# Performance work log

Hardware: AMD Instinct MI355X
Metric: run time of the kernel (lower is better)

Reference implementation:

```python
import jax, jax.numpy as jnp
import numpy as np

D_MODEL = 512
N_HEADS = 8
D_HEAD = D_MODEL // N_HEADS
N_LAYERS = 6
VOCAB = 32000
B, S = 4, 1024
EPS = 1e-5


def positional_encoding(length, d_model):
    # matches get_positional_encoding_table: pos * (1/10000**(i/d)), sin on even i, cos on odd i
    inv = 1.0 / (10000.0 ** (jnp.arange(d_model, dtype=jnp.float32) / d_model))
    ang = jnp.arange(length, dtype=jnp.float32)[:, None] * inv[None, :]  # [S, D]
    pe = jnp.where(jnp.arange(d_model) % 2 == 0, jnp.sin(ang), jnp.cos(ang))
    return pe


def layer_norm(x, g, b):
    m = jnp.mean(x, axis=-1, keepdims=True)
    v = jnp.mean((x - m) ** 2, axis=-1, keepdims=True)
    return (x - m) * jax.lax.rsqrt(v + EPS) * g + b


def setup_inputs() -> dict:
    key = jax.random.key(0)
    ks = jax.random.split(key, 9)
    sc = 0.02
    return {
        "tokens": jax.random.randint(ks[0], (B, S), 0, VOCAB),
        "emb": jax.random.normal(ks[1], (VOCAB, D_MODEL), jnp.float32) * sc,
        "Wq": jax.random.normal(ks[2], (N_LAYERS, D_MODEL, D_MODEL), jnp.float32) * sc,
        "bq": jnp.zeros((N_LAYERS, D_MODEL), jnp.float32),
        "Wk": jax.random.normal(ks[3], (N_LAYERS, D_MODEL, D_MODEL), jnp.float32) * sc,
        "bk": jnp.zeros((N_LAYERS, D_MODEL), jnp.float32),
        "Wv": jax.random.normal(ks[4], (N_LAYERS, D_MODEL, D_MODEL), jnp.float32) * sc,
        "bv": jnp.zeros((N_LAYERS, D_MODEL), jnp.float32),
        "Wo": jax.random.normal(ks[5], (N_LAYERS, D_MODEL, D_MODEL), jnp.float32) * sc,
        "bo": jnp.zeros((N_LAYERS, D_MODEL), jnp.float32),
        "W1": jax.random.normal(ks[6], (N_LAYERS, D_MODEL, 4 * D_MODEL), jnp.float32) * sc,
        "b1": jnp.zeros((N_LAYERS, 4 * D_MODEL), jnp.float32),
        "W2": jax.random.normal(ks[7], (N_LAYERS, 4 * D_MODEL, D_MODEL), jnp.float32) * sc,
        "b2": jnp.zeros((N_LAYERS, D_MODEL), jnp.float32),
        "ln_g": jnp.ones((N_LAYERS, D_MODEL), jnp.float32),
        "ln_b": jnp.zeros((N_LAYERS, D_MODEL), jnp.float32),
    }


def encoder_layer(x, Wq, bq, Wk, bk, Wv, bv, Wo, bo, W1, b1, W2, b2, g, b):
    bsz = x.shape[0]
    q = (x @ Wq + bq).reshape(bsz, -1, N_HEADS, D_HEAD).transpose(0, 2, 1, 3)  # [B,h,S,dk]
    k = (x @ Wk + bk).reshape(bsz, -1, N_HEADS, D_HEAD).transpose(0, 2, 1, 3)
    v = (x @ Wv + bv).reshape(bsz, -1, N_HEADS, D_HEAD).transpose(0, 2, 1, 3)
    scores = jnp.einsum('bhqd,bhkd->bhqk', q, k) / (D_HEAD ** 0.5)
    w = jax.nn.softmax(scores, axis=-1)
    attn = jnp.einsum('bhqk,bhkd->bhqd', w, v)  # [B,h,S,dv]
    # faithful to source bug: .view(B,-1,h*dv) WITHOUT transposing heads back
    attn = attn.reshape(bsz, -1, N_HEADS * D_HEAD)  # [B,S,D] with heads/seq interleaved
    x = layer_norm(x + (attn @ Wo + bo), g, b)
    ffn = jnp.maximum(x @ W1 + b1, 0.0) @ W2 + b2
    x = layer_norm(x + ffn, g, b)  # same (shared) LayerNorm params, as in source
    return x


def reference(tokens, emb, Wq, bq, Wk, bk, Wv, bv, Wo, bo, W1, b1, W2, b2, ln_g, ln_b):
    x = emb[tokens]  # [B,S,D]
    x = x + positional_encoding(x.shape[1], D_MODEL)
    for i in range(N_LAYERS):
        x = encoder_layer(x, Wq[i], bq[i], Wk[i], bk[i], Wv[i], bv[i], Wo[i], bo[i],
                          W1[i], b1[i], W2[i], b2[i], ln_g[i], ln_b[i])
    return x
```

## Files before the change

kernel.cpp:

```cpp
#include <hip/hip_runtime.h>
#include <hip/hip_bf16.h>
#include <math.h>

typedef unsigned short ushort_t;
typedef unsigned int uint_t;
typedef __attribute__((ext_vector_type(8))) short bfrag_t;
typedef __attribute__((ext_vector_type(4))) float facc_t;
typedef __attribute__((ext_vector_type(16))) float facc16_t;

#define D_MODEL 512
#define NH 8
#define DH 64
#define NL 6
#define BB 4
#define SS 1024
#define ROWS (BB*SS)
#define DFF 2048

__device__ inline ushort_t f2bf(float f) {
    __hip_bfloat16 h = __float2bfloat16(f);
    return *(ushort_t*)&h;
}
__device__ inline float bf2f(ushort_t u) {
    unsigned int x = ((unsigned int)u) << 16;
    union { unsigned int i; float f; } c; c.i = x;
    return c.f;
}
__device__ inline uint_t pkbf(float lo, float hi) {
    return (uint_t)f2bf(lo) | ((uint_t)f2bf(hi) << 16);
}
__device__ inline void gload_lds16(const void* g, void* l) {
    __builtin_amdgcn_global_load_lds((const __attribute__((address_space(1))) unsigned int*)g,
                                     (__attribute__((address_space(3))) unsigned int*)l, 16, 0, 0);
}

__global__ __launch_bounds__(256) void embed_pe(const int* __restrict__ tok,
                                                const float* __restrict__ emb,
                                                float* __restrict__ x,
                                                ushort_t* __restrict__ xbf) {
    int row = blockIdx.x;
    int s = row & (SS - 1);
    int t = tok[row];
    const float* e = emb + (size_t)t * D_MODEL;
    for (int i = threadIdx.x; i < D_MODEL; i += 256) {
        float freq = __expf(-9.210340371976184f * ((float)i / (float)D_MODEL));
        float ang = (float)s * freq;
        float pe = (i & 1) ? cosf(ang) : sinf(ang);
        float v = e[i] + pe;
        x[(size_t)row * D_MODEL + i] = v;
        xbf[(size_t)row * D_MODEL + i] = f2bf(v);
    }
}

__global__ __launch_bounds__(256) void prep_weights(const float* __restrict__ Wq,
                                                    const float* __restrict__ Wk,
                                                    const float* __restrict__ Wv,
                                                    const float* __restrict__ Wo,
                                                    const float* __restrict__ W1,
                                                    const float* __restrict__ W2,
                                                    int layer, ushort_t* __restrict__ wlay) {
    __shared__ float tile[32][33];
    int z = blockIdx.z;
    const float* src; ushort_t* dst; int K, N;
    size_t o512 = (size_t)layer * 512 * 512;
    size_t o1M  = (size_t)layer * 512 * 2048;
    switch (z) {
        case 0: src = Wq + o512; dst = wlay;               K = 512;  N = 512;  break;
        case 1: src = Wk + o512; dst = wlay + 262144;      K = 512;  N = 512;  break;
        case 2: src = Wv + o512; dst = wlay + 524288;      K = 512;  N = 512;  break;
        case 3: src = Wo + o512; dst = wlay + 786432;      K = 512;  N = 512;  break;
        case 4: src = W1 + o1M;  dst = wlay + 1048576;     K = 512;  N = 2048; break;
        default:src = W2 + o1M;  dst = wlay + 2097152;     K = 2048; N = 512;  break;
    }
    int n0 = blockIdx.x * 32, k0 = blockIdx.y * 32;
    if (n0 >= N || k0 >= K) return;
    int tx = threadIdx.x & 31, ty = threadIdx.x >> 5;
    #pragma unroll
    for (int i = 0; i < 4; i++)
        tile[ty + i * 8][tx] = src[(size_t)(k0 + ty + i * 8) * N + n0 + tx];
    __syncthreads();
    #pragma unroll
    for (int i = 0; i < 4; i++)
        dst[(size_t)(n0 + ty + i * 8) * K + k0 + tx] = f2bf(tile[tx][ty + i * 8]);
}

__global__ __launch_bounds__(256) void concat_bias(const float* __restrict__ bq,
                                                   const float* __restrict__ bk,
                                                   const float* __restrict__ bv,
                                                   float* __restrict__ bqkv) {
    int l = blockIdx.x;
    for (int i = threadIdx.x; i < 1536; i += 256) {
        float v = (i < 512) ? bq[l * 512 + i]
                : (i < 1024) ? bk[l * 512 + i - 512]
                : bv[l * 512 + i - 1024];
        bqkv[l * 1536 + i] = v;
    }
}

template<int BM, int BN, int SPLIT>
__global__ __launch_bounds__(256) void gemm_pipe(const ushort_t* __restrict__ A,
                                                 const ushort_t* __restrict__ Bt,
                                                 const float* __restrict__ bias,
                                                 float* __restrict__ Cf,
                                                 ushort_t* __restrict__ Cb0,
                                                 ushort_t* __restrict__ Cb1,
                                                 int N, int Ktot, int relu) {
    constexpr int TI = BM / 32, TJ = BN / 32;
    __shared__ ushort_t lA[2][BM * 64];
    __shared__ ushort_t lB[2][BN * 64];

    const int tid = threadIdx.x;
    const int w = tid >> 6, lane = tid & 63;
    const int wr = w & 1, wc = w >> 1;
    const int lane16 = lane & 15, quad = lane >> 4;
    const int row0 = blockIdx.y * BM, col0 = blockIdx.x * BN;
    const int kz = (SPLIT > 1) ? blockIdx.z : 0;
    const int Ks = Ktot / SPLIT;
    const int kbeg = kz * Ks;

    facc_t acc[TI][TJ];
    #pragma unroll
    for (int i = 0; i < TI; i++)
        #pragma unroll
        for (int j = 0; j < TJ; j++)
            acc[i][j] = (facc_t){0.f, 0.f, 0.f, 0.f};

    auto stage = [&](int buf, int k0) {
        #pragma unroll
        for (int i = 0; i < BM / 32; i++) {
            int g = i * 256 + tid;
            int r = g >> 3, p = g & 7;
            int q = p ^ (r & 7);
            gload_lds16(A + (size_t)(row0 + r) * Ktot + kbeg + k0 + q * 8,
                        lA[buf] + (size_t)g * 8);
        }
        #pragma unroll
        for (int i = 0; i < BN / 32; i++) {
            int g = i * 256 + tid;
            int r = g >> 3, p = g & 7;
            int q = p ^ (r & 7);
            gload_lds16(Bt + (size_t)(col0 + r) * Ktot + kbeg + k0 + q * 8,
                        lB[buf] + (size_t)g * 8);
        }
    };
    auto compute = [&](int buf) {
        #pragma unroll
        for (int kk = 0; kk < 2; kk++) {
            bfrag_t af[TI], bf_[TJ];
            int q = kk * 4 + quad;
            #pragma unroll
            for (int t = 0; t < TI; t++) {
                int m = wr * (BM / 2) + t * 16 + lane16;
                af[t] = *(const bfrag_t*)(lA[buf] + ((size_t)m * 8 + (q ^ (m & 7))) * 8);
            }
            #pragma unroll
            for (int t = 0; t < TJ; t++) {
                int n = wc * (BN / 2) + t * 16 + lane16;
                bf_[t] = *(const bfrag_t*)(lB[buf] + ((size_t)n * 8 + (q ^ (n & 7))) * 8);
            }
            #pragma unroll
            for (int ti = 0; ti < TI; ti++)
                #pragma unroll
                for (int tj = 0; tj < TJ; tj++)
                    acc[ti][tj] = __builtin_amdgcn_mfma_f32_16x16x32_bf16(
                        af[ti], bf_[tj], acc[ti][tj], 0, 0, 0);
        }
    };

    const int nt = Ks >> 6;
    stage(0, 0);
    __syncthreads();
    for (int t = 0; t < nt; t++) {
        if (t + 1 < nt) stage((t + 1) & 1, (t + 1) * 64);
        compute(t & 1);
        __syncthreads();
    }

    float bv_[TJ];
    #pragma unroll
    for (int tj = 0; tj < TJ; tj++)
        bv_[tj] = (SPLIT > 1 && kz != 0) ? 0.f
                 : bias[col0 + wc * (BN / 2) + tj * 16 + lane16];

    ushort_t* Cb = (SPLIT > 1 && kz != 0) ? Cb1 : Cb0;

    #pragma unroll
    for (int ti = 0; ti < TI; ti++) {
        int grow = row0 + wr * (BM / 2) + ti * 16 + quad * 4;
        #pragma unroll
        for (int tj = 0; tj < TJ; tj++) {
            int gcol = col0 + wc * (BN / 2) + tj * 16 + lane16;
            #pragma unroll
            for (int rr = 0; rr < 4; rr++) {
                float v = acc[ti][tj][rr] + bv_[tj];
                if (relu) v = fmaxf(v, 0.f);
                size_t idx = (size_t)(grow + rr) * N + gcol;
                if (Cf) Cf[idx] = v;
                if (Cb) Cb[idx] = f2bf(v);
            }
        }
    }
}

__global__ __launch_bounds__(128) void attn_mfma_split(const ushort_t* __restrict__ qkv,
                                                       ushort_t* __restrict__ Yp,
                                                       float2* __restrict__ mlp) {
    __shared__ __align__(16) ushort_t lK[4096];
    __shared__ __align__(16) ushort_t lVT[2][4096];

    const int tid = threadIdx.x;
    const int w = tid >> 6, lane = tid & 63;
    const int l31 = lane & 31, H = lane >> 5;
    const int qt = blockIdx.x, h = blockIdx.y;
    const int b = blockIdx.z >> 1, kh = blockIdx.z & 1;
    const int kt0 = kh * 8;

    const float LOG2E = 1.4426950408889634f;
    const float SC = 0.125f * 1.4426950408889634f;

    const ushort_t* Qrow = qkv + (size_t)(b * SS + qt * 64 + w * 32 + l31) * 1536 + h * 64;
    bfrag_t qb[4];
    #pragma unroll
    for (int s = 0; s < 4; s++)
        qb[s] = *(const bfrag_t*)(Qrow + s * 16 + H * 8);

    facc16_t O0, O1;
    #pragma unroll
    for (int r = 0; r < 16; r++) { O0[r] = 0.f; O1[r] = 0.f; }
    float mrow = -INFINITY, lrow = 0.f;

    const int vkey = tid & 63;
    const int vdg  = tid >> 6;
    const int vk8 = vkey >> 3, vj = vkey & 7;

    auto stageK = [&](int kt) {
        #pragma unroll
        for (int i = 0; i < 4; i++) {
            int g = i * 128 + tid;
            int r = g >> 3, p = g & 7;
            int q = p ^ (r & 7);
            gload_lds16(qkv + (size_t)(b * SS + kt * 64 + r) * 1536 + h * 64 + 512 + q * 8,
                        lK + (size_t)g * 8);
        }
    };
    auto loadV = [&](int kt, ushort_t* vs) {
        const ushort_t* vsrc = qkv + (size_t)(b * SS + kt * 64 + vkey) * 1536
                               + h * 64 + 1024 + vdg * 32;
        #pragma unroll
        for (int i4 = 0; i4 < 4; i4++)
            *(uint4*)(vs + i4 * 8) = *(const uint4*)(vsrc + i4 * 8);
    };
    auto writeV = [&](const ushort_t* vs, int buf) {
        #pragma unroll
        for (int e = 0; e < 32; e++) {
            int n = vdg * 32 + e;
            lVT[buf][(size_t)(n * 8 + (vk8 ^ (n & 7))) * 8 + vj] = vs[e];
        }
    };

    {
        ushort_t v0[32];
        stageK(kt0);
        loadV(kt0, v0);
        writeV(v0, 0);
    }
    __syncthreads();

    for (int kt = kt0; kt < kt0 + 8; kt++) {
        const int buf = (kt - kt0) & 1;
        const bool more = (kt < kt0 + 7);

        ushort_t vn[32];
        if (more) loadV(kt + 1, vn);

        facc16_t sfv[2];
        #pragma unroll
        for (int half = 0; half < 2; half++) {
            facc16_t s_;
            #pragma unroll
            for (int r = 0; r < 16; r++) s_[r] = 0.f;
            int row = half * 32 + l31;
            #pragma unroll
            for (int s = 0; s < 4; s++) {
                int c = 2 * s + H;
                bfrag_t kf = *(const bfrag_t*)(lK + ((size_t)row * 8 + (c ^ (row & 7))) * 8);
                s_ = __builtin_amdgcn_mfma_f32_32x32x16_bf16(kf, qb[s], s_, 0, 0, 0);
            }
            sfv[half] = s_;
        }

        if (more) {
            __syncthreads();
            stageK(kt + 1);
        }

        #pragma unroll
        for (int half = 0; half < 2; half++) {
            facc16_t s_ = sfv[half];

            float mt = s_[0];
            #pragma unroll
            for (int r = 1; r < 16; r++) mt = fmaxf(mt, s_[r]);
            mt *= 0.125f;
            mt = fmaxf(mt, __shfl_xor(mt, 32));

            bool small = (mt <= mrow + 8.f);
            if (!__all(small)) {
                float mn = fmaxf(mrow, mt);
                float al = __builtin_amdgcn_exp2f((mrow - mn) * LOG2E);
                mrow = mn;
                lrow *= al;
                #pragma unroll
                for (int r = 0; r < 16; r++) { O0[r] *= al; O1[r] *= al; }
            }
            float mC = mrow * LOG2E;

            float p[16];
            float ps = 0.f;
            #pragma unroll
            for (int r = 0; r < 16; r++) {
                p[r] = __builtin_amdgcn_exp2f(fmaf(s_[r], SC, -mC));
                ps += p[r];
            }
            ps += __shfl_xor(ps, 32);
            lrow += ps;

            uint_t A0 = pkbf(p[0], p[1]),   A1 = pkbf(p[2], p[3]);
            uint_t B0 = pkbf(p[4], p[5]),   B1 = pkbf(p[6], p[7]);
            uint_t C0 = pkbf(p[8], p[9]),   C1 = pkbf(p[10], p[11]);
            uint_t D0 = pkbf(p[12], p[13]), D1 = pkbf(p[14], p[15]);
            uint_t XA0 = __shfl_xor(A0, 32), XA1 = __shfl_xor(A1, 32);
            uint_t XB0 = __shfl_xor(B0, 32), XB1 = __shfl_xor(B1, 32);
            uint_t XC0 = __shfl_xor(C0, 32), XC1 = __shfl_xor(C1, 32);
            uint_t XD0 = __shfl_xor(D0, 32), XD1 = __shfl_xor(D1, 32);

            union { bfrag_t v; uint_t u[4]; } pf0, pf1;
            pf0.u[0] = H ? XB0 : A0;  pf0.u[1] = H ? XB1 : A1;
            pf0.u[2] = H ? B0 : XA0;  pf0.u[3] = H ? B1 : XA1;
            pf1.u[0] = H ? XD0 : C0;  pf1.u[1] = H ? XD1 : C1;
            pf1.u[2] = H ? D0 : XC0;  pf1.u[3] = H ? D1 : XC1;

            #pragma unroll
            for (int t = 0; t < 2; t++) {
                int n = 32 * t + l31;
                #pragma unroll
                for (int ks = 0; ks < 2; ks++) {
                    int c = half * 4 + 2 * ks + H;
                    bfrag_t vf = *(const bfrag_t*)(&lVT[buf][((size_t)n * 8 + (c ^ (n & 7))) * 8]);
                    if (t == 0)
                        O0 = __builtin_amdgcn_mfma_f32_32x32x16_bf16(
                            vf, ks ? pf1.v : pf0.v, O0, 0, 0, 0);
                    else
                        O1 = __builtin_amdgcn_mfma_f32_32x32x16_bf16(
                            vf, ks ? pf1.v : pf0.v, O1, 0, 0, 0);
                }
            }
        }

        if (more) writeV(vn, buf ^ 1);

        __syncthreads();
    }

    size_t rbase = ((size_t)(kh * BB + b) * NH + h) * SS + qt * 64 + w * 32 + l31;
    float inv = 1.f / lrow;
    #pragma unroll
    for (int t = 0; t < 2; t++) {
        #pragma unroll
        for (int g = 0; g < 4; g++) {
            float v0 = (t ? O1[4 * g]     : O0[4 * g])     * inv;
            float v1 = (t ? O1[4 * g + 1] : O0[4 * g + 1]) * inv;
            float v2 = (t ? O1[4 * g + 2] : O0[4 * g + 2]) * inv;
            float v3 = (t ? O1[4 * g + 3] : O0[4 * g + 3]) * inv;
            uint2 pkd = make_uint2(pkbf(v0, v1), pkbf(v2, v3));
            *(uint2*)(Yp + rbase * DH + 32 * t + 8 * g + 4 * H) = pkd;
        }
    }
    if (H == 0)
        mlp[rbase] = make_float2(mrow, lrow);
}

__global__ __launch_bounds__(256) void attn_combine(const ushort_t* __restrict__ Yp,
                                                    const float2* __restrict__ mlp,
                                                    ushort_t* __restrict__ ab) {
    const float LOG2E = 1.4426950408889634f;
    int rid = blockIdx.x * 32 + (threadIdx.x >> 3);
    int d0 = (threadIdx.x & 7) * 8;
    float2 ml0 = mlp[rid];
    float2 ml1 = mlp[32768 + rid];
    float m = fmaxf(ml0.x, ml1.x);
    float a0 = __builtin_amdgcn_exp2f((ml0.x - m) * LOG2E) * ml0.y;
    float a1 = __builtin_amdgcn_exp2f((ml1.x - m) * LOG2E) * ml1.y;
    float inv = 1.f / (a0 + a1);
    a0 *= inv; a1 *= inv;
    uint4 u0 = *(const uint4*)(Yp + (size_t)rid * DH + d0);
    uint4 u1 = *(const uint4*)(Yp + (size_t)32768 * DH + (size_t)rid * DH + d0);
    const ushort_t* p0 = (const ushort_t*)&u0;
    const ushort_t* p1 = (const ushort_t*)&u1;
    ushort_t o[8];
    #pragma unroll
    for (int e = 0; e < 8; e++)
        o[e] = f2bf(a0 * bf2f(p0[e]) + a1 * bf2f(p1[e]));
    *(uint4*)(ab + (size_t)rid * DH + d0) = *(uint4*)o;
}

template<int NP>
__global__ __launch_bounds__(256) void add_lnb(const float* __restrict__ x,
                                               const ushort_t* __restrict__ d0,
                                               const ushort_t* __restrict__ d1,
                                               const float* __restrict__ g,
                                               const float* __restrict__ bparm,
                                               float* __restrict__ outf,
                                               ushort_t* __restrict__ outb) {
    __shared__ float red[2][4];
    int row = blockIdx.x;
    int t = threadIdx.x;
    const float* xr = x + (size_t)row * D_MODEL;
    const ushort_t* dr0 = d0 + (size_t)row * D_MODEL;
    float del0 = bf2f(dr0[t]);
    float del1 = bf2f(dr0[t + 256]);
    if (NP == 2) {
        const ushort_t* dr1 = d1 + (size_t)row * D_MODEL;
        del0 += bf2f(dr1[t]);
        del1 += bf2f(dr1[t + 256]);
    }
    float v0 = xr[t] + del0;
    float v1 = xr[t + 256] + del1;
    float s = v0 + v1;
    float ss = v0 * v0 + v1 * v1;
    #pragma unroll
    for (int off = 1; off < 64; off <<= 1) {
        s  += __shfl_xor(s, off);
        ss += __shfl_xor(ss, off);
    }
    int lane = t & 63, wid = t >> 6;
    if (lane == 0) { red[0][wid] = s; red[1][wid] = ss; }
    __syncthreads();
    s  = red[0][0] + red[0][1] + red[0][2] + red[0][3];
    ss = red[1][0] + red[1][1] + red[1][2] + red[1][3];
    float mean = s * (1.f / D_MODEL);
    float var = ss * (1.f / D_MODEL) - mean * mean;
    float rinv = rsqrtf(var + 1e-5f);
    float o0 = (v0 - mean) * rinv * g[t]       + bparm[t];
    float o1 = (v1 - mean) * rinv * g[t + 256] + bparm[t + 256];
    float* orow = outf + (size_t)row * D_MODEL;
    orow[t] = o0; orow[t + 256] = o1;
    ushort_t* brow = outb + (size_t)row * D_MODEL;
    brow[t] = f2bf(o0); brow[t + 256] = f2bf(o1);
}

extern "C" void kernel_launch(void* const* d_in, const int* in_sizes, int n_in,
                              void* d_out, int out_size, void* d_ws, size_t ws_size,
                              hipStream_t stream) {
    const int* tokens = (const int*)d_in[0];
    const float* emb = (const float*)d_in[1];
    const float* Wq = (const float*)d_in[2];  const float* bq = (const float*)d_in[3];
    const float* Wk = (const float*)d_in[4];  const float* bk = (const float*)d_in[5];
    const float* Wv = (const float*)d_in[6];  const float* bv = (const float*)d_in[7];
    const float* Wo = (const float*)d_in[8];  const float* bo = (const float*)d_in[9];
    const float* W1 = (const float*)d_in[10]; const float* b1 = (const float*)d_in[11];
    const float* W2 = (const float*)d_in[12]; const float* b2 = (const float*)d_in[13];
    const float* lng = (const float*)d_in[14]; const float* lnb = (const float*)d_in[15];

    char* base = (char*)d_ws;
    ushort_t* wlay = (ushort_t*)(base);
    float*    bqkv = (float*)   (base + 6291456);
    float*    x    = (float*)   (base + 6328320);
    ushort_t* xbf  = (ushort_t*)(base + 14716928);
    float*    tmp  = (float*)   (base + 18911232);
    ushort_t* qkv  = (ushort_t*)(base + 27299840);
    ushort_t* ab   = (ushort_t*)(base + 39882752);
    ushort_t* mid  = qkv;

    ushort_t* Yp   = (ushort_t*)tmp;
    float2*   mlp  = (float2*)xbf;
    ushort_t* dlt0 = (ushort_t*)tmp;
    ushort_t* dlt1 = (ushort_t*)tmp + 2097152;

    ushort_t* wqkv_t = wlay;
    ushort_t* wo_t   = wlay + 786432;
    ushort_t* w1_t   = wlay + 1048576;
    ushort_t* w2_t   = wlay + 2097152;

    concat_bias<<<NL, 256, 0, stream>>>(bq, bk, bv, bqkv);
    embed_pe<<<ROWS, 256, 0, stream>>>(tokens, emb, x, xbf);

    for (int l = 0; l < NL; l++) {
        prep_weights<<<dim3(64, 64, 6), 256, 0, stream>>>(Wq, Wk, Wv, Wo, W1, W2, l, wlay);

        gemm_pipe<128, 64, 1><<<dim3(24, 32), 256, 0, stream>>>(
            xbf, wqkv_t, bqkv + l * 1536, nullptr, qkv, nullptr, 1536, 512, 0);

        attn_mfma_split<<<dim3(16, NH, BB * 2), 128, 0, stream>>>(qkv, Yp, mlp);
        attn_combine<<<1024, 256, 0, stream>>>(Yp, mlp, ab);

        gemm_pipe<64, 64, 1><<<dim3(8, 64), 256, 0, stream>>>(
            ab, wo_t, bo + l * D_MODEL, nullptr, dlt0, nullptr, 512, 512, 0);
        add_lnb<1><<<ROWS, 256, 0, stream>>>(x, dlt0, nullptr,
                                             lng + l * D_MODEL, lnb + l * D_MODEL,
                                             x, xbf);

        gemm_pipe<128, 128, 1><<<dim3(16, 32), 256, 0, stream>>>(
            xbf, w1_t, b1 + l * DFF, nullptr, mid, nullptr, 2048, 512, 1);

        gemm_pipe<64, 64, 2><<<dim3(8, 64, 2), 256, 0, stream>>>(
            mid, w2_t, b2 + l * D_MODEL, nullptr, dlt0, dlt1, 512, 2048, 0);

        float* lnout = (l == NL - 1) ? (float*)d_out : x;
        add_lnb<2><<<ROWS, 256, 0, stream>>>(x, dlt0, dlt1,
                                             lng + l * D_MODEL, lnb + l * D_MODEL,
                                             lnout, xbf);
    }
}
```

Before: 856.5 us.

## Split attention key range four ways and combine partials in a four-way merge

After: 887.2 us. +3.6%, slower.

```diff
diff --git a/kernel.cpp b/kernel.cpp
--- a/kernel.cpp
+++ b/kernel.cpp
@@ -202,18 +202,21 @@
     }
 }
 
-__global__ __launch_bounds__(128) void attn_mfma_split(const ushort_t* __restrict__ qkv,
-                                                       ushort_t* __restrict__ Yp,
-                                                       float2* __restrict__ mlp) {
+__global__ __launch_bounds__(128) void attn_mfma_split4(const ushort_t* __restrict__ qkv,
+                                                        ushort_t* __restrict__ Yp0,
+                                                        ushort_t* __restrict__ Yp1,
+                                                        ushort_t* __restrict__ Yp2,
+                                                        ushort_t* __restrict__ Yp3,
+                                                        float2* __restrict__ mlp) {
     __shared__ __align__(16) ushort_t lK[4096];
-    __shared__ __align__(16) ushort_t lVT[2][4096];
+    __shared__ __align__(16) ushort_t lVT[4096];
 
     const int tid = threadIdx.x;
     const int w = tid >> 6, lane = tid & 63;
     const int l31 = lane & 31, H = lane >> 5;
     const int qt = blockIdx.x, h = blockIdx.y;
-    const int b = blockIdx.z >> 1, kh = blockIdx.z & 1;
-    const int kt0 = kh * 8;
+    const int b = blockIdx.z >> 2, kh = blockIdx.z & 3;
+    const int kt0 = kh * 4;
 
     const float LOG2E = 1.4426950408889634f;
     const float SC = 0.125f * 1.4426950408889634f;
@@ -250,11 +253,11 @@
         for (int i4 = 0; i4 < 4; i4++)
             *(uint4*)(vs + i4 * 8) = *(const uint4*)(vsrc + i4 * 8);
     };
-    auto writeV = [&](const ushort_t* vs, int buf) {
+    auto writeV = [&](const ushort_t* vs) {
         #pragma unroll
         for (int e = 0; e < 32; e++) {
             int n = vdg * 32 + e;
-            lVT[buf][(size_t)(n * 8 + (vk8 ^ (n & 7))) * 8 + vj] = vs[e];
+            lVT[(size_t)(n * 8 + (vk8 ^ (n & 7))) * 8 + vj] = vs[e];
         }
     };
 
@@ -262,18 +265,18 @@
         ushort_t v0[32];
         stageK(kt0);
         loadV(kt0, v0);
-        writeV(v0, 0);
+        writeV(v0);
     }
     __syncthreads();
 
-    for (int kt = kt0; kt < kt0 + 8; kt++) {
-        const int buf = (kt - kt0) & 1;
-        const bool more = (kt < kt0 + 7);
+    for (int kt = kt0; kt < kt0 + 4; kt++) {
+        const bool more = (kt < kt0 + 3);
 
         ushort_t vn[32];
         if (more) loadV(kt + 1, vn);
 
         facc16_t sfv[2];
+        __builtin_amdgcn_s_setprio(1);
         #pragma unroll
         for (int half = 0; half < 2; half++) {
             facc16_t s_;
@@ -288,6 +291,7 @@
             }
             sfv[half] = s_;
         }
+        __builtin_amdgcn_s_setprio(0);
 
         if (more) {
             __syncthreads();
@@ -298,10 +302,12 @@
         for (int half = 0; half < 2; half++) {
             facc16_t s_ = sfv[half];
 
-            float mt = s_[0];
-            #pragma unroll
-            for (int r = 1; r < 16; r++) mt = fmaxf(mt, s_[r]);
-            mt *= 0.125f;
+            float t0 = fmaxf(s_[0], s_[1]),   t1 = fmaxf(s_[2], s_[3]);
+            float t2 = fmaxf(s_[4], s_[5]),   t3 = fmaxf(s_[6], s_[7]);
+            float t4 = fmaxf(s_[8], s_[9]),   t5 = fmaxf(s_[10], s_[11]);
+            float t6 = fmaxf(s_[12], s_[13]), t7 = fmaxf(s_[14], s_[15]);
+            float mt = fmaxf(fmaxf(fmaxf(t0, t1), fmaxf(t2, t3)),
+                             fmaxf(fmaxf(t4, t5), fmaxf(t6, t7))) * 0.125f;
             mt = fmaxf(mt, __shfl_xor(mt, 32));
 
             bool small = (mt <= mrow + 8.f);
@@ -316,12 +322,14 @@
             float mC = mrow * LOG2E;
 
             float p[16];
-            float ps = 0.f;
-            #pragma unroll
-            for (int r = 0; r < 16; r++) {
+            #pragma unroll
+            for (int r = 0; r < 16; r++)
                 p[r] = __builtin_amdgcn_exp2f(fmaf(s_[r], SC, -mC));
-                ps += p[r];
-            }
+            float u0 = p[0] + p[1],   u1 = p[2] + p[3];
+            float u2 = p[4] + p[5],   u3 = p[6] + p[7];
+            float u4 = p[8] + p[9],   u5 = p[10] + p[11];
+            float u6 = p[12] + p[13], u7 = p[14] + p[15];
+            float ps = ((u0 + u1) + (u2 + u3)) + ((u4 + u5) + (u6 + u7));
             ps += __shfl_xor(ps, 32);
             lrow += ps;
 
@@ -340,13 +348,14 @@
             pf1.u[0] = H ? XD0 : C0;  pf1.u[1] = H ? XD1 : C1;
             pf1.u[2] = H ? D0 : XC0;  pf1.u[3] = H ? D1 : XC1;
 
+            __builtin_amdgcn_s_setprio(1);
             #pragma unroll
             for (int t = 0; t < 2; t++) {
                 int n = 32 * t + l31;
                 #pragma unroll
                 for (int ks = 0; ks < 2; ks++) {
                     int c = half * 4 + 2 * ks + H;
-                    bfrag_t vf = *(const bfrag_t*)(&lVT[buf][((size_t)n * 8 + (c ^ (n & 7))) * 8]);
+                    bfrag_t vf = *(const bfrag_t*)(lVT + ((size_t)n * 8 + (c ^ (n & 7))) * 8);
                     if (t == 0)
                         O0 = __builtin_amdgcn_mfma_f32_32x32x16_bf16(
                             vf, ks ? pf1.v : pf0.v, O0, 0, 0, 0);
@@ -355,14 +364,17 @@
                             vf, ks ? pf1.v : pf0.v, O1, 0, 0, 0);
                 }
             }
-        }
-
-        if (more) writeV(vn, buf ^ 1);
-
-        __syncthreads();
-    }
-
-    size_t rbase = ((size_t)(kh * BB + b) * NH + h) * SS + qt * 64 + w * 32 + l31;
+            __builtin_amdgcn_s_setprio(0);
+        }
+
+        if (more) {
+            __syncthreads();
+            writeV(vn);
+        }
+    }
+
+    ushort_t* Ypz = (kh == 0) ? Yp0 : (kh == 1) ? Yp1 : (kh == 2) ? Yp2 : Yp3;
+    size_t rbase = ((size_t)b * NH + h) * SS + qt * 64 + w * 32 + l31;
     float inv = 1.f / lrow;
     #pragma unroll
     for (int t = 0; t < 2; t++) {
@@ -373,35 +385,48 @@
             float v2 = (t ? O1[4 * g + 2] : O0[4 * g + 2]) * inv;
             float v3 = (t ? O1[4 * g + 3] : O0[4 * g + 3]) * inv;
             uint2 pkd = make_uint2(pkbf(v0, v1), pkbf(v2, v3));
-            *(uint2*)(Yp + rbase * DH + 32 * t + 8 * g + 4 * H) = pkd;
+            *(uint2*)(Ypz + rbase * DH + 32 * t + 8 * g + 4 * H) = pkd;
         }
     }
     if (H == 0)
-        mlp[rbase] = make_float2(mrow, lrow);
-}
-
-__global__ __launch_bounds__(256) void attn_combine(const ushort_t* __restrict__ Yp,
-                                                    const float2* __restrict__ mlp,
-                                                    ushort_t* __restrict__ ab) {
+        mlp[(size_t)kh * 32768 + rbase] = make_float2(mrow, lrow);
+}
+
+__global__ __launch_bounds__(256) void attn_combine4(const ushort_t* __restrict__ Y0,
+                                                     const ushort_t* __restrict__ Y1,
+                                                     const ushort_t* __restrict__ Y2,
+                                                     const ushort_t* __restrict__ Y3,
+                                                     const float2* __restrict__ mlp,
+                                                     ushort_t* __restrict__ ab) {
     const float LOG2E = 1.4426950408889634f;
     int rid = blockIdx.x * 32 + (threadIdx.x >> 3);
     int d0 = (threadIdx.x & 7) * 8;
     float2 ml0 = mlp[rid];
     float2 ml1 = mlp[32768 + rid];
-    float m = fmaxf(ml0.x, ml1.x);
+    float2 ml2 = mlp[65536 + rid];
+    float2 ml3 = mlp[98304 + rid];
+    float m = fmaxf(fmaxf(ml0.x, ml1.x), fmaxf(ml2.x, ml3.x));
     float a0 = __builtin_amdgcn_exp2f((ml0.x - m) * LOG2E) * ml0.y;
     float a1 = __builtin_amdgcn_exp2f((ml1.x - m) * LOG2E) * ml1.y;
-    float inv = 1.f / (a0 + a1);
-    a0 *= inv; a1 *= inv;
-    uint4 u0 = *(const uint4*)(Yp + (size_t)rid * DH + d0);
-    uint4 u1 = *(const uint4*)(Yp + (size_t)32768 * DH + (size_t)rid * DH + d0);
+    float a2 = __builtin_amdgcn_exp2f((ml2.x - m) * LOG2E) * ml2.y;
+    float a3 = __builtin_amdgcn_exp2f((ml3.x - m) * LOG2E) * ml3.y;
+    float inv = 1.f / (((a0 + a1) + (a2 + a3)));
+    a0 *= inv; a1 *= inv; a2 *= inv; a3 *= inv;
+    size_t off = (size_t)rid * DH + d0;
+    uint4 u0 = *(const uint4*)(Y0 + off);
+    uint4 u1 = *(const uint4*)(Y1 + off);
+    uint4 u2 = *(const uint4*)(Y2 + off);
+    uint4 u3 = *(const uint4*)(Y3 + off);
     const ushort_t* p0 = (const ushort_t*)&u0;
     const ushort_t* p1 = (const ushort_t*)&u1;
+    const ushort_t* p2 = (const ushort_t*)&u2;
+    const ushort_t* p3 = (const ushort_t*)&u3;
     ushort_t o[8];
     #pragma unroll
     for (int e = 0; e < 8; e++)
-        o[e] = f2bf(a0 * bf2f(p0[e]) + a1 * bf2f(p1[e]));
-    *(uint4*)(ab + (size_t)rid * DH + d0) = *(uint4*)o;
+        o[e] = f2bf((a0 * bf2f(p0[e]) + a1 * bf2f(p1[e]))
+                  + (a2 * bf2f(p2[e]) + a3 * bf2f(p3[e])));
+    *(uint4*)(ab + off) = *(uint4*)o;
 }
 
 template<int NP>
@@ -472,8 +497,11 @@
     ushort_t* ab   = (ushort_t*)(base + 39882752);
     ushort_t* mid  = qkv;
 
-    ushort_t* Yp   = (ushort_t*)tmp;
-    float2*   mlp  = (float2*)xbf;
+    ushort_t* Yp0  = (ushort_t*)tmp;
+    ushort_t* Yp1  = (ushort_t*)tmp + 2097152;
+    ushort_t* Yp2  = ab;
+    ushort_t* Yp3  = xbf;
+    float2*   mlp  = (float2*)wlay;
     ushort_t* dlt0 = (ushort_t*)tmp;
     ushort_t* dlt1 = (ushort_t*)tmp + 2097152;
 
@@ -491,8 +519,9 @@
         gemm_pipe<128, 64, 1><<<dim3(24, 32), 256, 0, stream>>>(
             xbf, wqkv_t, bqkv + l * 1536, nullptr, qkv, nullptr, 1536, 512, 0);
 
-        attn_mfma_split<<<dim3(16, NH, BB * 2), 128, 0, stream>>>(qkv, Yp, mlp);
-        attn_combine<<<1024, 256, 0, stream>>>(Yp, mlp, ab);
+        attn_mfma_split4<<<dim3(16, NH, BB * 4), 128, 0, stream>>>(
+            qkv, Yp0, Yp1, Yp2, Yp3, mlp);
+        attn_combine4<<<1024, 256, 0, stream>>>(Yp0, Yp1, Yp2, Yp3, mlp, ab);
 
         gemm_pipe<64, 64, 1><<<dim3(8, 64), 256, 0, stream>>>(
             ab, wo_t, bo + l * D_MODEL, nullptr, dlt0, nullptr, 512, 512, 0);
```

## Fuse split-attention combine into Wo GEMM and add MFMA priority hints

Applied to the files above, without the earlier changes.

Result: no change. 862.3 us (+0.7%).

```diff
diff --git a/kernel.cpp b/kernel.cpp
--- a/kernel.cpp
+++ b/kernel.cpp
@@ -202,6 +202,136 @@
     }
 }
 
+__global__ __launch_bounds__(256) void gemm_wo_fused(const ushort_t* __restrict__ Y,
+                                                     const float2* __restrict__ mlp,
+                                                     const ushort_t* __restrict__ Bt,
+                                                     const float* __restrict__ bias,
+                                                     ushort_t* __restrict__ Cb) {
+    __shared__ ushort_t lA[2][64 * 64];
+    __shared__ ushort_t lB[2][64 * 64];
+
+    const float LOG2E = 1.4426950408889634f;
+    const int tid = threadIdx.x;
+    const int w = tid >> 6, lane = tid & 63;
+    const int wr = w & 1, wc = w >> 1;
+    const int lane16 = lane & 15, quad = lane >> 4;
+    const int row0 = blockIdx.y * 64, col0 = blockIdx.x * 64;
+
+    facc_t acc[2][2];
+    #pragma unroll
+    for (int i = 0; i < 2; i++)
+        #pragma unroll
+        for (int j = 0; j < 2; j++)
+            acc[i][j] = (facc_t){0.f, 0.f, 0.f, 0.f};
+
+    auto stageB = [&](int buf, int k0) {
+        #pragma unroll
+        for (int i = 0; i < 2; i++) {
+            int g = i * 256 + tid;
+            int r = g >> 3, p = g & 7;
+            int q = p ^ (r & 7);
+            gload_lds16(Bt + (size_t)(col0 + r) * 512 + k0 + q * 8,
+                        lB[buf] + (size_t)g * 8);
+        }
+    };
+    auto issueA = [&](int k0, uint4* u0, uint4* u1, float2* m0, float2* m1) {
+        int hb = k0 >> 6;
+        #pragma unroll
+        for (int i = 0; i < 2; i++) {
+            int g = i * 256 + tid;
+            int r = g >> 3, p = g & 7;
+            int q = p ^ (r & 7);
+            int rid = (row0 + r) * 8 + hb;
+            m0[i] = mlp[rid];
+            m1[i] = mlp[32768 + rid];
+            size_t off = (size_t)rid * 64 + q * 8;
+            u0[i] = *(const uint4*)(Y + off);
+            u1[i] = *(const uint4*)(Y + 2097152 + off);
+        }
+    };
+    auto writeA = [&](int buf, const uint4* u0, const uint4* u1,
+                      const float2* m0, const float2* m1) {
+        #pragma unroll
+        for (int i = 0; i < 2; i++) {
+            int g = i * 256 + tid;
+            float mm = fmaxf(m0[i].x, m1[i].x);
+            float a0 = __builtin_amdgcn_exp2f((m0[i].x - mm) * LOG2E) * m0[i].y;
+            float a1 = __builtin_amdgcn_exp2f((m1[i].x - mm) * LOG2E) * m1[i].y;
+            float inv = 1.f / (a0 + a1);
+            a0 *= inv; a1 *= inv;
+            const ushort_t* p0 = (const ushort_t*)&u0[i];
+            const ushort_t* p1 = (const ushort_t*)&u1[i];
+            ushort_t o[8];
+            #pragma unroll
+            for (int e = 0; e < 8; e++)
+                o[e] = f2bf(a0 * bf2f(p0[e]) + a1 * bf2f(p1[e]));
+            *(uint4*)(lA[buf] + (size_t)g * 8) = *(uint4*)o;
+        }
+    };
+    auto compute = [&](int buf) {
+        #pragma unroll
+        for (int kk = 0; kk < 2; kk++) {
+            bfrag_t af[2], bf_[2];
+            int q = kk * 4 + quad;
+            #pragma unroll
+            for (int t = 0; t < 2; t++) {
+                int m = wr * 32 + t * 16 + lane16;
+                af[t] = *(const bfrag_t*)(lA[buf] + ((size_t)m * 8 + (q ^ (m & 7))) * 8);
+            }
+            #pragma unroll
+            for (int t = 0; t < 2; t++) {
+                int n = wc * 32 + t * 16 + lane16;
+                bf_[t] = *(const bfrag_t*)(lB[buf] + ((size_t)n * 8 + (q ^ (n & 7))) * 8);
+            }
+            #pragma unroll
+            for (int ti = 0; ti < 2; ti++)
+                #pragma unroll
+                for (int tj = 0; tj < 2; tj++)
+                    acc[ti][tj] = __builtin_amdgcn_mfma_f32_16x16x32_bf16(
+                        af[ti], bf_[tj], acc[ti][tj], 0, 0, 0);
+        }
+    };
+
+    {
+        uint4 u0[2], u1[2]; float2 m0[2], m1[2];
+        issueA(0, u0, u1, m0, m1);
+        stageB(0, 0);
+        writeA(0, u0, u1, m0, m1);
+    }
+    __syncthreads();
+
+    for (int t = 0; t < 8; t++) {
+        uint4 u0[2], u1[2]; float2 m0[2], m1[2];
+        const bool more = (t + 1 < 8);
+        if (more) {
+            stageB((t + 1) & 1, (t + 1) * 64);
+            issueA((t + 1) * 64, u0, u1, m0, m1);
+        }
+        compute(t & 1);
+        if (more) writeA((t + 1) & 1, u0, u1, m0, m1);
+        __syncthreads();
+    }
+
+    float bv_[2];
+    #pragma unroll
+    for (int tj = 0; tj < 2; tj++)
+        bv_[tj] = bias[col0 + wc * 32 + tj * 16 + lane16];
+
+    #pragma unroll
+    for (int ti = 0; ti < 2; ti++) {
+        int grow = row0 + wr * 32 + ti * 16 + quad * 4;
+        #pragma unroll
+        for (int tj = 0; tj < 2; tj++) {
+            int gcol = col0 + wc * 32 + tj * 16 + lane16;
+            #pragma unroll
+            for (int rr = 0; rr < 4; rr++) {
+                float v = acc[ti][tj][rr] + bv_[tj];
+                Cb[(size_t)(grow + rr) * 512 + gcol] = f2bf(v);
+            }
+        }
+    }
+}
+
 __global__ __launch_bounds__(128) void attn_mfma_split(const ushort_t* __restrict__ qkv,
                                                        ushort_t* __restrict__ Yp,
                                                        float2* __restrict__ mlp) {
@@ -274,6 +404,7 @@
         if (more) loadV(kt + 1, vn);
 
         facc16_t sfv[2];
+        __builtin_amdgcn_s_setprio(1);
         #pragma unroll
         for (int half = 0; half < 2; half++) {
             facc16_t s_;
@@ -288,6 +419,7 @@
             }
             sfv[half] = s_;
         }
+        __builtin_amdgcn_s_setprio(0);
 
         if (more) {
             __syncthreads();
@@ -298,10 +430,12 @@
         for (int half = 0; half < 2; half++) {
             facc16_t s_ = sfv[half];
 
-            float mt = s_[0];
-            #pragma unroll
-            for (int r = 1; r < 16; r++) mt = fmaxf(mt, s_[r]);
-            mt *= 0.125f;
+            float t0 = fmaxf(s_[0], s_[1]),   t1 = fmaxf(s_[2], s_[3]);
+            float t2 = fmaxf(s_[4], s_[5]),   t3 = fmaxf(s_[6], s_[7]);
+            float t4 = fmaxf(s_[8], s_[9]),   t5 = fmaxf(s_[10], s_[11]);
+            float t6 = fmaxf(s_[12], s_[13]), t7 = fmaxf(s_[14], s_[15]);
+            float mt = fmaxf(fmaxf(fmaxf(t0, t1), fmaxf(t2, t3)),
+                             fmaxf(fmaxf(t4, t5), fmaxf(t6, t7))) * 0.125f;
             mt = fmaxf(mt, __shfl_xor(mt, 32));
 
             bool small = (mt <= mrow + 8.f);
@@ -316,12 +450,14 @@
             float mC = mrow * LOG2E;
 
             float p[16];
-            float ps = 0.f;
-            #pragma unroll
-            for (int r = 0; r < 16; r++) {
+            #pragma unroll
+            for (int r = 0; r < 16; r++)
                 p[r] = __builtin_amdgcn_exp2f(fmaf(s_[r], SC, -mC));
-                ps += p[r];
-            }
+            float u0 = p[0] + p[1],   u1 = p[2] + p[3];
+            float u2 = p[4] + p[5],   u3 = p[6] + p[7];
+            float u4 = p[8] + p[9],   u5 = p[10] + p[11];
+            float u6 = p[12] + p[13], u7 = p[14] + p[15];
+            float ps = ((u0 + u1) + (u2 + u3)) + ((u4 + u5) + (u6 + u7));
             ps += __shfl_xor(ps, 32);
             lrow += ps;
 
@@ -340,6 +476,7 @@
             pf1.u[0] = H ? XD0 : C0;  pf1.u[1] = H ? XD1 : C1;
             pf1.u[2] = H ? D0 : XC0;  pf1.u[3] = H ? D1 : XC1;
 
+            __builtin_amdgcn_s_setprio(1);
             #pragma unroll
             for (int t = 0; t < 2; t++) {
                 int n = 32 * t + l31;
@@ -355,6 +492,7 @@
                             vf, ks ? pf1.v : pf0.v, O1, 0, 0, 0);
                 }
             }
+            __builtin_amdgcn_s_setprio(0);
         }
 
         if (more) writeV(vn, buf ^ 1);
@@ -378,30 +516,6 @@
     }
     if (H == 0)
         mlp[rbase] = make_float2(mrow, lrow);
-}
-
-__global__ __launch_bounds__(256) void attn_combine(const ushort_t* __restrict__ Yp,
-                                                    const float2* __restrict__ mlp,
-                                                    ushort_t* __restrict__ ab) {
-    const float LOG2E = 1.4426950408889634f;
-    int rid = blockIdx.x * 32 + (threadIdx.x >> 3);
-    int d0 = (threadIdx.x & 7) * 8;
-    float2 ml0 = mlp[rid];
-    float2 ml1 = mlp[32768 + rid];
-    float m = fmaxf(ml0.x, ml1.x);
-    float a0 = __builtin_amdgcn_exp2f((ml0.x - m) * LOG2E) * ml0.y;
-    float a1 = __builtin_amdgcn_exp2f((ml1.x - m) * LOG2E) * ml1.y;
-    float inv = 1.f / (a0 + a1);
-    a0 *= inv; a1 *= inv;
-    uint4 u0 = *(const uint4*)(Yp + (size_t)rid * DH + d0);
-    uint4 u1 = *(const uint4*)(Yp + (size_t)32768 * DH + (size_t)rid * DH + d0);
-    const ushort_t* p0 = (const ushort_t*)&u0;
-    const ushort_t* p1 = (const ushort_t*)&u1;
-    ushort_t o[8];
-    #pragma unroll
-    for (int e = 0; e < 8; e++)
-        o[e] = f2bf(a0 * bf2f(p0[e]) + a1 * bf2f(p1[e]));
-    *(uint4*)(ab + (size_t)rid * DH + d0) = *(uint4*)o;
 }
 
 template<int NP>
@@ -492,11 +606,10 @@
             xbf, wqkv_t, bqkv + l * 1536, nullptr, qkv, nullptr, 1536, 512, 0);
 
         attn_mfma_split<<<dim3(16, NH, BB * 2), 128, 0, stream>>>(qkv, Yp, mlp);
-        attn_combine<<<1024, 256, 0, stream>>>(Yp, mlp, ab);
-
-        gemm_pipe<64, 64, 1><<<dim3(8, 64), 256, 0, stream>>>(
-            ab, wo_t, bo + l * D_MODEL, nullptr, dlt0, nullptr, 512, 512, 0);
-        add_lnb<1><<<ROWS, 256, 0, stream>>>(x, dlt0, nullptr,
+
+        gemm_wo_fused<<<dim3(8, 64), 256, 0, stream>>>(
+            Yp, mlp, wo_t, bo + l * D_MODEL, ab);
+        add_lnb<1><<<ROWS, 256, 0, stream>>>(x, ab, nullptr,
                                              lng + l * D_MODEL, lnb + l * D_MODEL,
                                              x, xbf);
 
```
